# Kernel tuning notes

Measured on AMD Instinct MI355X. Metric: run time of the kernel, lower is better.

## Reference

```python
import math
import jax, jax.numpy as jnp
import numpy as np

NUM_HEADS = 8
FACTOR = 5


def setup_inputs() -> dict:
    key = jax.random.key(0)
    ks = jax.random.split(key, 7)
    B, L, D = 4, 2048, 512
    sample_k = min(FACTOR * int(math.ceil(math.log(L))), L)  # 40
    return {
        "q": jax.random.normal(ks[0], (B, L, D), dtype=jnp.float32),
        "k": jax.random.normal(ks[1], (B, L, D), dtype=jnp.float32),
        "v": jax.random.normal(ks[2], (B, L, D), dtype=jnp.float32),
        "Wq": jax.random.normal(ks[3], (D, D), dtype=jnp.float32) * (1.0 / math.sqrt(D)),
        "Wk": jax.random.normal(ks[4], (D, D), dtype=jnp.float32) * (1.0 / math.sqrt(D)),
        "Wv": jax.random.normal(ks[5], (D, D), dtype=jnp.float32) * (1.0 / math.sqrt(D)),
        # replaces tf.random.uniform((S, sample_k), maxval=L) shared over (B, H)
        "k_sample_idx": jax.random.randint(ks[6], (L, sample_k), 0, L, dtype=jnp.int32),
    }


def reference(q, k, v, Wq, Wk, Wv, k_sample_idx):
    B, L, D = q.shape
    H = NUM_HEADS
    E = D // H

    # dense_q / dense_k / dense_v (no bias)
    qp = q @ Wq
    kp = k @ Wk
    vp = v @ Wv

    # NOTE: original code uses a raw reshape (B, H, L, E), not a transpose-based
    # head split; we reproduce that exactly.
    q_ = qp.reshape(B, H, L, E)
    k_ = kp.reshape(B, H, L, E)
    v_ = vp.reshape(B, H, L, E)

    u_q = min(FACTOR * int(math.ceil(math.log(L))), L)  # top_n selected queries
    # sample_k is k_sample_idx.shape[-1]

    # --- _prob_qk: sparse sampled QK scores ---
    # k_sample[b,h,l,s,e] = k_[b,h, k_sample_idx[l,s], e]   (B,H,L,sample_k,E)
    k_sample = k_[:, :, k_sample_idx]
    qk_sample = jnp.einsum("bhle,bhlse->bhls", q_, k_sample)  # (B,H,L,sample_k)

    # sparsity measure: max - mean (mean uses /L as in original)
    m = jnp.max(qk_sample, axis=-1) - jnp.sum(qk_sample, axis=-1) / L  # (B,H,L)
    _, m_top = jax.lax.top_k(m, u_q)  # (B,H,u_q) indices of active queries

    # q_reduce = q_[b,h,m_top]  -> full scores against all keys
    q_reduce = jnp.take_along_axis(q_, m_top[..., None], axis=2)  # (B,H,u_q,E)
    scores = jnp.einsum("bhue,bhle->bhul", q_reduce, k_)  # (B,H,u_q,L)
    scores = scores * (1.0 / math.sqrt(D // H))

    # --- initial context: masked (causal) => cumulative sum of v ---
    context = jnp.cumsum(v_, axis=2)  # (B,H,L,E)

    # --- update context at selected query positions ---
    # ProbMask: key position j is masked iff j > original query index
    mask = jnp.arange(L)[None, None, None, :] > m_top[..., None]  # (B,H,u_q,L)
    scores = jnp.where(mask, -jnp.inf, scores)
    attn = jax.nn.softmax(scores, axis=-1)
    ctx_upd = jnp.einsum("bhul,bhle->bhue", attn, v_)  # (B,H,u_q,E)

    bidx = jnp.arange(B)[:, None, None]
    hidx = jnp.arange(H)[None, :, None]
    context = context.at[bidx, hidx, m_top].set(ctx_upd)

    return context.reshape(B, L, D)
```

## Files before the change

### kernel.cpp

```cpp
#include <hip/hip_runtime.h>
#include <hip/hip_bf16.h>
#include <float.h>

constexpr int Bc = 4;
constexpr int Lc = 2048;
constexpr int Dc = 512;
constexpr int Hc = 8;
constexpr int Ec = 64;
constexpr int Sc = 40;
constexpr int Uc = 40;
constexpr int LEc = Lc * Ec;
constexpr int BHc = Bc * Hc;
constexpr int Mrows = Bc * Lc;

typedef __attribute__((ext_vector_type(8))) short s16x8;
typedef __attribute__((ext_vector_type(4))) float f32x4;
typedef unsigned int u32;

__device__ __forceinline__ short f2bf(float x) {
    unsigned u = __float_as_uint(x);
    unsigned r = (u + 0x7fffu + ((u >> 16) & 1u)) >> 16;
    return (short)r;
}
__device__ __forceinline__ float bf2f(short s) {
    return __uint_as_float(((unsigned)(unsigned short)s) << 16);
}
__device__ __forceinline__ uint4 pack8(const short* s) {
    uint4 r;
    r.x = (unsigned)(unsigned short)s[0] | ((unsigned)(unsigned short)s[1] << 16);
    r.y = (unsigned)(unsigned short)s[2] | ((unsigned)(unsigned short)s[3] << 16);
    r.z = (unsigned)(unsigned short)s[4] | ((unsigned)(unsigned short)s[5] << 16);
    r.w = (unsigned)(unsigned short)s[6] | ((unsigned)(unsigned short)s[7] << 16);
    return r;
}

__device__ __forceinline__ void gld_lds16(const short* g, short* l) {
    __builtin_amdgcn_global_load_lds(
        (const __attribute__((address_space(1))) u32*)g,
        (__attribute__((address_space(3))) u32*)l, 16, 0, 0);
}

__global__ __launch_bounds__(256) void split_inputs(
    const float* __restrict__ q, const float* __restrict__ k, const float* __restrict__ v,
    short* __restrict__ qhi, short* __restrict__ qlo,
    short* __restrict__ khi, short* __restrict__ klo, short* __restrict__ vhi,
    int* __restrict__ cnt)
{
    int tid = blockIdx.x * 256 + threadIdx.x;
    if (tid < BHc) cnt[tid] = 0;
    int z   = tid >> 19;
    int g8  = tid & ((1 << 19) - 1);
    int row = g8 >> 6;
    int gin = g8 & 63;
    int slot = (gin & ~7) | ((gin ^ row) & 7);
    const float* src = (z == 0) ? q : (z == 1) ? k : v;
    const float4* s4 = (const float4*)src + (size_t)g8 * 2;
    float4 d0 = s4[0], d1 = s4[1];
    float f[8] = {d0.x, d0.y, d0.z, d0.w, d1.x, d1.y, d1.z, d1.w};
    short hs[8], ls[8];
    #pragma unroll
    for (int i = 0; i < 8; ++i) {
        hs[i] = f2bf(f[i]);
        ls[i] = f2bf(f[i] - bf2f(hs[i]));
    }
    size_t off = (size_t)row * 512 + slot * 8;
    if (z == 2) { *(uint4*)(vhi + off) = pack8(hs); return; }
    if (z == 0) { *(uint4*)(qhi + off) = pack8(hs); *(uint4*)(qlo + off) = pack8(ls); }
    else        { *(uint4*)(khi + off) = pack8(hs); *(uint4*)(klo + off) = pack8(ls); }
}

__global__ __launch_bounds__(256) void wprep(
    const float* __restrict__ Wq, const float* __restrict__ Wk,
    const float* __restrict__ Wv,
    short* __restrict__ Bq, short* __restrict__ Bk, short* __restrict__ Bv)
{
    __shared__ float tile[64][65];
    int z = blockIdx.z;
    const float* W = (z == 0) ? Wq : (z == 1) ? Wk : Wv;
    int k0 = blockIdx.x * 64, n0 = blockIdx.y * 64;
    int t = threadIdx.x;
    #pragma unroll
    for (int i = 0; i < 4; ++i) {
        int c = i * 256 + t, row = c >> 4, qq = c & 15;
        float4 d = *(const float4*)(W + (size_t)(k0 + row) * Dc + n0 + qq * 4);
        tile[row][qq * 4 + 0] = d.x; tile[row][qq * 4 + 1] = d.y;
        tile[row][qq * 4 + 2] = d.z; tile[row][qq * 4 + 3] = d.w;
    }
    __syncthreads();
    int n = t >> 2, ks = (t & 3) * 16;
    int nglob = n0 + n;
    short hs[16], ls[16];
    #pragma unroll
    for (int j = 0; j < 16; ++j) {
        float x = tile[ks + j][n];
        short h = f2bf(x);
        hs[j] = h;
        ls[j] = f2bf(x - bf2f(h));
    }
    int G0 = (k0 + ks) >> 3;
    int s0 = (G0 & ~7) | ((G0 ^ nglob) & 7);
    int s1 = ((G0 + 1) & ~7) | (((G0 + 1) ^ nglob) & 7);
    if (z < 2) {
        short* Bx = (z == 0) ? Bq : Bk;
        size_t rb = (size_t)nglob * 1536;
        *(uint4*)(Bx + rb + s0 * 8)        = pack8(hs);
        *(uint4*)(Bx + rb + s1 * 8)        = pack8(hs + 8);
        *(uint4*)(Bx + rb + 512 + s0 * 8)  = pack8(ls);
        *(uint4*)(Bx + rb + 512 + s1 * 8)  = pack8(ls + 8);
        *(uint4*)(Bx + rb + 1024 + s0 * 8) = pack8(hs);
        *(uint4*)(Bx + rb + 1024 + s1 * 8) = pack8(hs + 8);
    } else {
        size_t rb = (size_t)nglob * 512;
        *(uint4*)(Bv + rb + s0 * 8) = pack8(hs);
        *(uint4*)(Bv + rb + s1 * 8) = pack8(hs + 8);
    }
}

__global__ __launch_bounds__(256) void gemm_mfma(
    const short* __restrict__ qhi, const short* __restrict__ qlo,
    const short* __restrict__ khi, const short* __restrict__ klo,
    const short* __restrict__ vhi,
    const short* __restrict__ Bq, const short* __restrict__ Bk,
    const short* __restrict__ Bv,
    float* __restrict__ qp, float* __restrict__ kp, float* __restrict__ vp)
{
    int z = blockIdx.z;
    const short* Ahi = (z == 0) ? qhi : (z == 1) ? khi : vhi;
    const short* Alo = (z == 0) ? qlo : (z == 1) ? klo : vhi;
    const short* Bx  = (z == 0) ? Bq  : (z == 1) ? Bk  : Bv;
    float* O = (z == 0) ? qp : (z == 1) ? kp : vp;
    const int Ktot = (z == 2) ? 512 : 1536;
    const int nseg = (z == 2) ? 1 : 3;

    __shared__ short As[128 * 64];
    __shared__ short Bs[128 * 64];

    const int t = threadIdx.x;
    const int lane = t & 63, w = t >> 6;
    const int wm = w >> 1, wn = w & 1;
    const int row0 = blockIdx.x * 128, col0 = blockIdx.y * 128;
    const int kg = lane >> 4, fr = lane & 15;
    const int sx = fr & 7;
    const int lrow = lane >> 3, lcol = (lane & 7) * 8;

    f32x4 acc[4][4];
    #pragma unroll
    for (int i = 0; i < 4; ++i)
        #pragma unroll
        for (int j = 0; j < 4; ++j)
            acc[i][j] = (f32x4){0.f, 0.f, 0.f, 0.f};

    for (int seg = 0; seg < nseg; ++seg) {
        const short* Asrc = ((seg == 2) ? Alo : Ahi)
                          + (size_t)(row0 + lrow) * 512 + lcol;
        const short* Bsrc = Bx + (size_t)(col0 + lrow) * Ktot + seg * 512 + lcol;
        for (int ks = 0; ks < 512; ks += 64) {
            __syncthreads();
            #pragma unroll
            for (int i = 0; i < 4; ++i) {
                int r = w * 32 + i * 8;
                gld_lds16(Asrc + (size_t)r * 512 + ks, &As[r * 64]);
            }
            #pragma unroll
            for (int i = 0; i < 4; ++i) {
                int r = w * 32 + i * 8;
                gld_lds16(Bsrc + (size_t)r * Ktot + ks, &Bs[r * 64]);
            }
            __syncthreads();

            #pragma unroll
            for (int kk = 0; kk < 2; ++kk) {
                const int slot = ((kk * 4 + kg) ^ sx) * 8;
                s16x8 a[4];
                #pragma unroll
                for (int mi = 0; mi < 4; ++mi)
                    a[mi] = *(const s16x8*)&As[(wm * 64 + mi * 16 + fr) * 64 + slot];
                #pragma unroll
                for (int ni = 0; ni < 4; ++ni) {
                    s16x8 b = *(const s16x8*)&Bs[(wn * 64 + ni * 16 + fr) * 64 + slot];
                    #pragma unroll
                    for (int mi = 0; mi < 4; ++mi)
                        acc[mi][ni] = __builtin_amdgcn_mfma_f32_16x16x32_bf16(a[mi], b, acc[mi][ni], 0, 0, 0);
                }
            }
        }
    }

    #pragma unroll
    for (int mi = 0; mi < 4; ++mi) {
        #pragma unroll
        for (int ni = 0; ni < 4; ++ni) {
            int row = row0 + wm * 64 + mi * 16 + (lane >> 4) * 4;
            int col = col0 + wn * 64 + ni * 16 + (lane & 15);
            #pragma unroll
            for (int r4 = 0; r4 < 4; ++r4)
                O[(size_t)(row + r4) * Dc + col] = acc[mi][ni][r4];
        }
    }
}

__global__ __launch_bounds__(256) void compute_m(
    const float* __restrict__ qp, const float* __restrict__ kp,
    const int* __restrict__ ksi, float* __restrict__ m_out)
{
    __shared__ float qsh[4][Ec];
    __shared__ int   jsh[4][Sc];
    int w    = threadIdx.x >> 6;
    int lane = threadIdx.x & 63;
    int xcd  = blockIdx.x & 7;
    int i    = blockIdx.x >> 3;
    int bh   = (xcd << 2) | (i >> 9);
    int l    = (i & 511) * 4 + w;
    const float* kbase = kp + (size_t)bh * LEc;

    qsh[w][lane] = qp[(size_t)bh * LEc + l * Ec + lane];
    if (lane < Sc) jsh[w][lane] = ksi[l * Sc + lane];
    __syncthreads();

    const int g = lane >> 2;
    const int c = lane & 3;

    float mx = -FLT_MAX, sm = 0.f;
    #pragma unroll
    for (int it = 0; it < 3; ++it) {
        int s = it * 16 + g;
        bool valid = (s < Sc);
        float partial = 0.f;
        if (valid) {
            int j = jsh[w][s];
            const float4* krow = (const float4*)(kbase + (size_t)j * Ec);
            #pragma unroll
            for (int ii = 0; ii < 4; ++ii) {
                float4 kv = krow[ii * 4 + c];
                float4 qv = *(const float4*)&qsh[w][ii * 16 + c * 4];
                partial += kv.x * qv.x + kv.y * qv.y + kv.z * qv.z + kv.w * qv.w;
            }
        }
        partial += __shfl_xor(partial, 1);
        partial += __shfl_xor(partial, 2);
        float vmax = valid ? partial : -FLT_MAX;
        float vsum = (valid && c == 0) ? partial : 0.f;
        #pragma unroll
        for (int o = 4; o < 64; o <<= 1) {
            vmax = fmaxf(vmax, __shfl_xor(vmax, o));
            vsum += __shfl_xor(vsum, o);
        }
        mx = fmaxf(mx, vmax);
        sm += vsum;
    }
    if (lane == 0) m_out[bh * Lc + l] = mx - sm * (1.0f / Lc);
}

__global__ __launch_bounds__(256) void topk40(
    const float* __restrict__ m_in, int* __restrict__ mtop, int* __restrict__ cnt)
{
    __shared__ float vals[Lc];
    int bh = blockIdx.x >> 3, seg = blockIdx.x & 7;
    int t = threadIdx.x;
    for (int i = t; i < Lc; i += 256) vals[i] = m_in[bh * Lc + i];
    __syncthreads();
    int myi = seg * 256 + t;
    float vi = vals[myi];
    int g0 = 0, g1 = 0, g2 = 0, g3 = 0;
    int e0 = 0, e1 = 0, e2 = 0, e3 = 0;
    const float4* v4 = (const float4*)vals;
    #pragma unroll 4
    for (int j4 = 0; j4 < Lc / 4; ++j4) {
        float4 vv = v4[j4];
        g0 += (vv.x > vi);  e0 += (vv.x >= vi);
        g1 += (vv.y > vi);  e1 += (vv.y >= vi);
        g2 += (vv.z > vi);  e2 += (vv.z >= vi);
        g3 += (vv.w > vi);  e3 += (vv.w >= vi);
    }
    int rgt = g0 + g1 + g2 + g3;
    int rge = e0 + e1 + e2 + e3;
    bool sel;
    if (rge <= Uc)      sel = true;
    else if (rgt >= Uc) sel = false;
    else {
        int req = 0;
        for (int j = 0; j < myi; ++j) req += (vals[j] == vi);
        sel = (rgt + req) < Uc;
    }
    if (sel) {
        int pos = atomicAdd(&cnt[bh], 1);
        mtop[bh * Uc + pos] = myi;
    }
}

constexpr int CH = 64;
constexpr int CR = 32;

__global__ __launch_bounds__(64) void cumsum_p1(
    const float* __restrict__ vp, float* __restrict__ psum)
{
    int bid = blockIdx.x;
    int e = threadIdx.x;
    int bh = bid >> 6, ch = bid & 63;
    const float* base = vp + (size_t)bh * LEc + (ch * CR) * Ec + e;
    float s = 0.f;
    #pragma unroll 8
    for (int r = 0; r < CR; ++r) s += base[r * Ec];
    psum[(size_t)bid * Ec + e] = s;
}

__global__ __launch_bounds__(64) void cumsum_p2(float* __restrict__ psum)
{
    int bh = blockIdx.x;
    int e = threadIdx.x;
    float off = 0.f;
    for (int c = 0; c < CH; ++c) {
        size_t idx = (size_t)(bh * CH + c) * Ec + e;
        float tv = psum[idx];
        psum[idx] = off;
        off += tv;
    }
}

__global__ __launch_bounds__(64) void cumsum_p3(
    const float* __restrict__ vp, const float* __restrict__ psum,
    float* __restrict__ out)
{
    int bid = blockIdx.x;
    int e = threadIdx.x;
    int bh = bid >> 6, ch = bid & 63;
    const float* base = vp  + (size_t)bh * LEc + (ch * CR) * Ec + e;
    float*       ob   = out + (size_t)bh * LEc + (ch * CR) * Ec + e;
    float run = psum[(size_t)bid * Ec + e];
    #pragma unroll 8
    for (int r = 0; r < CR; ++r) { run += base[r * Ec]; ob[r * Ec] = run; }
}

constexpr int ACH = 16;
constexpr int AROWS = 128;

__global__ __launch_bounds__(512) void attn_partial(
    const float* __restrict__ qp, const float* __restrict__ kp,
    const float* __restrict__ vp, const int* __restrict__ mtop,
    float* __restrict__ pl, float* __restrict__ pacc)
{
    __shared__ float Kt[64][68];
    __shared__ float Vt[64][68];
    __shared__ float qsh[40][64];
    __shared__ float p_t[40][68];
    __shared__ int   lsel_sh[40];

    int half = blockIdx.x >> 8, sub = blockIdx.x & 255;
    int bh = sub & 31;
    int ch = half ? (15 - (sub >> 5)) : (sub >> 5);
    int t = threadIdx.x, w = t >> 6, lane = t & 63;
    const float* kb = kp + (size_t)bh * LEc;
    const float* vb = vp + (size_t)bh * LEc;

    if (t < Uc) lsel_sh[t] = mtop[bh * Uc + t];
    __syncthreads();
    for (int i = t; i < Uc * Ec; i += 512) {
        int u = i >> 6, e = i & 63;
        qsh[u][e] = qp[(size_t)bh * LEc + lsel_sh[u] * Ec + e];
    }

    const int u0 = w * 5;
    float acc[5]  = {0.f, 0.f, 0.f, 0.f, 0.f};
    float lreg[5] = {0.f, 0.f, 0.f, 0.f, 0.f};

    for (int tt = 0; tt < AROWS / 64; ++tt) {
        int l0 = ch * AROWS + tt * 64;
        __syncthreads();
        #pragma unroll
        for (int i = 0; i < 2; ++i) {
            int f = i * 512 + t, row = f >> 4, cg = f & 15;
            *(float4*)&Kt[row][cg * 4] = *(const float4*)(kb + (size_t)(l0 + row) * Ec + cg * 4);
            *(float4*)&Vt[row][cg * 4] = *(const float4*)(vb + (size_t)(l0 + row) * Ec + cg * 4);
        }
        __syncthreads();

        int gl = l0 + lane;
        float4 kr[16];
        #pragma unroll
        for (int i = 0; i < 16; ++i) kr[i] = *(const float4*)&Kt[lane][i * 4];

        bool act[5];
        #pragma unroll
        for (int j = 0; j < 5; ++j) {
            int u = u0 + j, ls = lsel_sh[u];
            act[j] = (l0 <= ls);
            if (!act[j]) continue;
            float p = 0.f;
            if (gl <= ls) {
                float dot = 0.f;
                #pragma unroll
                for (int i = 0; i < 16; ++i) {
                    float4 qv = *(const float4*)&qsh[u][i * 4];
                    dot += kr[i].x * qv.x + kr[i].y * qv.y + kr[i].z * qv.z + kr[i].w * qv.w;
                }
                p = __expf(dot * 0.125f);
            }
            p_t[u][lane] = p;
            float ps = p;
            #pragma unroll
            for (int o = 1; o < 64; o <<= 1) ps += __shfl_xor(ps, o);
            lreg[j] += ps;
        }

        #pragma unroll
        for (int i = 0; i < 16; ++i) {
            float v0 = Vt[i * 4 + 0][lane];
            float v1 = Vt[i * 4 + 1][lane];
            float v2 = Vt[i * 4 + 2][lane];
            float v3 = Vt[i * 4 + 3][lane];
            #pragma unroll
            for (int j = 0; j < 5; ++j) {
                if (!act[j]) continue;
                float4 pv = *(const float4*)&p_t[u0 + j][i * 4];
                acc[j] += pv.x * v0 + pv.y * v1 + pv.z * v2 + pv.w * v3;
            }
        }
    }

    #pragma unroll
    for (int j = 0; j < 5; ++j) {
        size_t idx = ((size_t)bh * ACH + ch) * Uc + u0 + j;
        if (lane == 0) pl[idx] = lreg[j];
        pacc[idx * Ec + lane] = acc[j];
    }
}

__global__ __launch_bounds__(256) void attn_combine(
    const float* __restrict__ pl, const float* __restrict__ pacc,
    const int* __restrict__ mtop, float* __restrict__ out)
{
    int wid = blockIdx.x * 4 + (threadIdx.x >> 6);
    int lane = threadIdx.x & 63;
    int bh = wid / Uc, u = wid % Uc;
    float l = 0.f, a = 0.f;
    for (int i = 0; i < ACH; ++i) {
        size_t idx = ((size_t)bh * ACH + i) * Uc + u;
        l += pl[idx];
        a += pacc[idx * Ec + lane];
    }
    int lsel = mtop[bh * Uc + u];
    out[(size_t)bh * LEc + lsel * Ec + lane] = a / l;
}

extern "C" void kernel_launch(void* const* d_in, const int* in_sizes, int n_in,
                              void* d_out, int out_size, void* d_ws, size_t ws_size,
                              hipStream_t stream)
{
    const float* q   = (const float*)d_in[0];
    const float* k   = (const float*)d_in[1];
    const float* v   = (const float*)d_in[2];
    const float* Wq  = (const float*)d_in[3];
    const float* Wk  = (const float*)d_in[4];
    const float* Wv  = (const float*)d_in[5];
    const int*   ksi = (const int*)d_in[6];
    float* out = (float*)d_out;

    float* wsf  = (float*)d_ws;
    float* qp   = wsf;
    float* kp   = qp + (size_t)Mrows * Dc;
    float* vp   = kp + (size_t)Mrows * Dc;
    float* psum = vp + (size_t)Mrows * Dc;
    float* m_ws = psum + (size_t)BHc * CH * Ec;
    int*   mtop = (int*)(m_ws + (size_t)BHc * Lc);
    short* qhi = (short*)(mtop + BHc * Uc);
    short* qlo = qhi + (size_t)Mrows * Dc;
    short* khi = qlo + (size_t)Mrows * Dc;
    short* klo = khi + (size_t)Mrows * Dc;
    short* vhi = klo + (size_t)Mrows * Dc;
    short* Bq  = vhi + (size_t)Mrows * Dc;
    short* Bk  = Bq + (size_t)Dc * 1536;
    short* Bv  = Bk + (size_t)Dc * 1536;
    float* pl  = (float*)(Bv + (size_t)Dc * 512);
    float* pacc = pl + (size_t)BHc * ACH * Uc;
    int*   cnt  = (int*)(pacc + (size_t)BHc * ACH * Uc * Ec);

    split_inputs<<<3 * (Mrows * Dc / 8) / 256, 256, 0, stream>>>(
        q, k, v, qhi, qlo, khi, klo, vhi, cnt);
    wprep<<<dim3(8, 8, 3), 256, 0, stream>>>(Wq, Wk, Wv, Bq, Bk, Bv);

    dim3 g1(Mrows / 128, Dc / 128, 3);
    gemm_mfma<<<g1, 256, 0, stream>>>(qhi, qlo, khi, klo, vhi, Bq, Bk, Bv,
                                      qp, kp, vp);

    compute_m<<<(BHc * Lc) / 4, 256, 0, stream>>>(qp, kp, ksi, m_ws);

    topk40<<<BHc * 8, 256, 0, stream>>>(m_ws, mtop, cnt);

    attn_partial<<<BHc * ACH, 512, 0, stream>>>(qp, kp, vp, mtop, pl, pacc);

    cumsum_p1<<<BHc * CH, 64, 0, stream>>>(vp, psum);
    cumsum_p2<<<BHc, 64, 0, stream>>>(psum);
    cumsum_p3<<<BHc * CH, 64, 0, stream>>>(vp, psum, out);

    attn_combine<<<BHc * Uc / 4, 256, 0, stream>>>(pl, pacc, mtop, out);
}
```

Baseline: 151.4 us.

## Reuse A tile across hi/lo B segments in split-bf16 GEMM; parallelize cumsum scan

The split-precision projection GEMM now loads the A-hi tile once and multiplies it against both the B-hi and B-lo tiles in the same pass, then does a second pass for A-lo times B-hi. This drops the redundant third copy of B-hi from weight prep and cuts A-tile global loads and syncs, at the cost of an extra LDS buffer. The cumsum offset pass is changed from a serial loop over 64 chunks by one wave per head to a wave-level shuffle scan with many more blocks, which removes a serial dependency chain.

```diff
diff --git a/kernel.cpp b/kernel.cpp
--- a/kernel.cpp
+++ b/kernel.cpp
@@ -107,8 +107,6 @@
         *(uint4*)(Bx + rb + s1 * 8)        = pack8(hs + 8);
         *(uint4*)(Bx + rb + 512 + s0 * 8)  = pack8(ls);
         *(uint4*)(Bx + rb + 512 + s1 * 8)  = pack8(ls + 8);
-        *(uint4*)(Bx + rb + 1024 + s0 * 8) = pack8(hs);
-        *(uint4*)(Bx + rb + 1024 + s1 * 8) = pack8(hs + 8);
     } else {
         size_t rb = (size_t)nglob * 512;
         *(uint4*)(Bv + rb + s0 * 8) = pack8(hs);
@@ -129,11 +127,11 @@
     const short* Alo = (z == 0) ? qlo : (z == 1) ? klo : vhi;
     const short* Bx  = (z == 0) ? Bq  : (z == 1) ? Bk  : Bv;
     float* O = (z == 0) ? qp : (z == 1) ? kp : vp;
-    const int Ktot = (z == 2) ? 512 : 1536;
-    const int nseg = (z == 2) ? 1 : 3;
+    const int BKt = (z == 2) ? 512 : 1536;
 
     __shared__ short As[128 * 64];
-    __shared__ short Bs[128 * 64];
+    __shared__ short Bh[128 * 64];
+    __shared__ short Bl[128 * 64];
 
     const int t = threadIdx.x;
     const int lane = t & 63, w = t >> 6;
@@ -150,24 +148,29 @@
         for (int j = 0; j < 4; ++j)
             acc[i][j] = (f32x4){0.f, 0.f, 0.f, 0.f};
 
-    for (int seg = 0; seg < nseg; ++seg) {
-        const short* Asrc = ((seg == 2) ? Alo : Ahi)
-                          + (size_t)(row0 + lrow) * 512 + lcol;
-        const short* Bsrc = Bx + (size_t)(col0 + lrow) * Ktot + seg * 512 + lcol;
+    const short* AhiS = Ahi + (size_t)(row0 + lrow) * 512 + lcol;
+    const short* AloS = Alo + (size_t)(row0 + lrow) * 512 + lcol;
+    const short* BhiS = Bx + (size_t)(col0 + lrow) * BKt + lcol;
+
+    if (z < 2) {
         for (int ks = 0; ks < 512; ks += 64) {
             __syncthreads();
             #pragma unroll
             for (int i = 0; i < 4; ++i) {
                 int r = w * 32 + i * 8;
-                gld_lds16(Asrc + (size_t)r * 512 + ks, &As[r * 64]);
-            }
-            #pragma unroll
-            for (int i = 0; i < 4; ++i) {
-                int r = w * 32 + i * 8;
-                gld_lds16(Bsrc + (size_t)r * Ktot + ks, &Bs[r * 64]);
+                gld_lds16(AhiS + (size_t)r * 512 + ks, &As[r * 64]);
+            }
+            #pragma unroll
+            for (int i = 0; i < 4; ++i) {
+                int r = w * 32 + i * 8;
+                gld_lds16(BhiS + (size_t)r * 1536 + ks, &Bh[r * 64]);
+            }
+            #pragma unroll
+            for (int i = 0; i < 4; ++i) {
+                int r = w * 32 + i * 8;
+                gld_lds16(BhiS + (size_t)r * 1536 + 512 + ks, &Bl[r * 64]);
             }
             __syncthreads();
-
             #pragma unroll
             for (int kk = 0; kk < 2; ++kk) {
                 const int slot = ((kk * 4 + kg) ^ sx) * 8;
@@ -177,10 +180,73 @@
                     a[mi] = *(const s16x8*)&As[(wm * 64 + mi * 16 + fr) * 64 + slot];
                 #pragma unroll
                 for (int ni = 0; ni < 4; ++ni) {
-                    s16x8 b = *(const s16x8*)&Bs[(wn * 64 + ni * 16 + fr) * 64 + slot];
+                    s16x8 bh = *(const s16x8*)&Bh[(wn * 64 + ni * 16 + fr) * 64 + slot];
+                    s16x8 bl = *(const s16x8*)&Bl[(wn * 64 + ni * 16 + fr) * 64 + slot];
                     #pragma unroll
                     for (int mi = 0; mi < 4; ++mi)
-                        acc[mi][ni] = __builtin_amdgcn_mfma_f32_16x16x32_bf16(a[mi], b, acc[mi][ni], 0, 0, 0);
+                        acc[mi][ni] = __builtin_amdgcn_mfma_f32_16x16x32_bf16(a[mi], bh, acc[mi][ni], 0, 0, 0);
+                    #pragma unroll
+                    for (int mi = 0; mi < 4; ++mi)
+                        acc[mi][ni] = __builtin_amdgcn_mfma_f32_16x16x32_bf16(a[mi], bl, acc[mi][ni], 0, 0, 0);
+                }
+            }
+        }
+        for (int ks = 0; ks < 512; ks += 64) {
+            __syncthreads();
+            #pragma unroll
+            for (int i = 0; i < 4; ++i) {
+                int r = w * 32 + i * 8;
+                gld_lds16(AloS + (size_t)r * 512 + ks, &As[r * 64]);
+            }
+            #pragma unroll
+            for (int i = 0; i < 4; ++i) {
+                int r = w * 32 + i * 8;
+                gld_lds16(BhiS + (size_t)r * 1536 + ks, &Bh[r * 64]);
+            }
+            __syncthreads();
+            #pragma unroll
+            for (int kk = 0; kk < 2; ++kk) {
+                const int slot = ((kk * 4 + kg) ^ sx) * 8;
+                s16x8 a[4];
+                #pragma unroll
+                for (int mi = 0; mi < 4; ++mi)
+                    a[mi] = *(const s16x8*)&As[(wm * 64 + mi * 16 + fr) * 64 + slot];
+                #pragma unroll
+                for (int ni = 0; ni < 4; ++ni) {
+                    s16x8 bh = *(const s16x8*)&Bh[(wn * 64 + ni * 16 + fr) * 64 + slot];
+                    #pragma unroll
+                    for (int mi = 0; mi < 4; ++mi)
+                        acc[mi][ni] = __builtin_amdgcn_mfma_f32_16x16x32_bf16(a[mi], bh, acc[mi][ni], 0, 0, 0);
+                }
+            }
+        }
+    } else {
+        for (int ks = 0; ks < 512; ks += 64) {
+            __syncthreads();
+            #pragma unroll
+            for (int i = 0; i < 4; ++i) {
+                int r = w * 32 + i * 8;
+                gld_lds16(AhiS + (size_t)r * 512 + ks, &As[r * 64]);
+            }
+            #pragma unroll
+            for (int i = 0; i < 4; ++i) {
+                int r = w * 32 + i * 8;
+                gld_lds16(BhiS + (size_t)r * 512 + ks, &Bh[r * 64]);
+            }
+            __syncthreads();
+            #pragma unroll
+            for (int kk = 0; kk < 2; ++kk) {
+                const int slot = ((kk * 4 + kg) ^ sx) * 8;
+                s16x8 a[4];
+                #pragma unroll
+                for (int mi = 0; mi < 4; ++mi)
+                    a[mi] = *(const s16x8*)&As[(wm * 64 + mi * 16 + fr) * 64 + slot];
+                #pragma unroll
+                for (int ni = 0; ni < 4; ++ni) {
+                    s16x8 bh = *(const s16x8*)&Bh[(wn * 64 + ni * 16 + fr) * 64 + slot];
+                    #pragma unroll
+                    for (int mi = 0; mi < 4; ++mi)
+                        acc[mi][ni] = __builtin_amdgcn_mfma_f32_16x16x32_bf16(a[mi], bh, acc[mi][ni], 0, 0, 0);
                 }
             }
         }
@@ -304,17 +370,21 @@
     psum[(size_t)bid * Ec + e] = s;
 }
 
-__global__ __launch_bounds__(64) void cumsum_p2(float* __restrict__ psum)
-{
-    int bh = blockIdx.x;
-    int e = threadIdx.x;
-    float off = 0.f;
-    for (int c = 0; c < CH; ++c) {
-        size_t idx = (size_t)(bh * CH + c) * Ec + e;
-        float tv = psum[idx];
-        psum[idx] = off;
-        off += tv;
-    }
+__global__ __launch_bounds__(256) void cumsum_p2(float* __restrict__ psum)
+{
+    int wid  = blockIdx.x * 4 + (threadIdx.x >> 6);
+    int lane = threadIdx.x & 63;
+    int bh = wid >> 6, e = wid & 63;
+    size_t idx = (size_t)(bh * CH + lane) * Ec + e;
+    float v = psum[idx];
+    #pragma unroll
+    for (int off = 1; off < 64; off <<= 1) {
+        float u = __shfl_up(v, off);
+        v += (lane >= off) ? u : 0.f;
+    }
+    float ex = __shfl_up(v, 1);
+    if (lane == 0) ex = 0.f;
+    psum[idx] = ex;
 }
 
 __global__ __launch_bounds__(64) void cumsum_p3(
@@ -489,7 +559,7 @@
     attn_partial<<<BHc * ACH, 512, 0, stream>>>(qp, kp, vp, mtop, pl, pacc);
 
     cumsum_p1<<<BHc * CH, 64, 0, stream>>>(vp, psum);
-    cumsum_p2<<<BHc, 64, 0, stream>>>(psum);
+    cumsum_p2<<<(BHc * Ec) / 4, 256, 0, stream>>>(psum);
     cumsum_p3<<<BHc * CH, 64, 0, stream>>>(vp, psum, out);
 
     attn_combine<<<BHc * Uc / 4, 256, 0, stream>>>(pl, pacc, mtop, out);
```

Result: slower. 157.0 us (+3.7%).
